# Performance work log

Hardware: AMD Instinct MI355X
Metric: run time of the kernel (lower is better)

Reference implementation:

```python
import jax, jax.numpy as jnp
import numpy as np

VOCAB, EMB, HID = 32000, 512, 1024

def setup_inputs() -> dict:
    key = jax.random.key(0)
    k1, k2, k3, k4, k5, k6 = jax.random.split(key, 6)
    s_e = 1.0 / np.sqrt(EMB)
    s_h = 1.0 / np.sqrt(HID)
    return {
        "x": jax.random.randint(k1, (32, 512), 0, VOCAB, dtype=jnp.int64),
        "emb_table": jax.random.normal(k2, (VOCAB, EMB), dtype=jnp.float32),
        "W_ih": jax.random.uniform(k3, (4 * HID, EMB), jnp.float32, -s_h, s_h),
        "W_hh": jax.random.uniform(k4, (4 * HID, HID), jnp.float32, -s_h, s_h),
        "b_ih": jax.random.uniform(k5, (4 * HID,), jnp.float32, -s_h, s_h),
        "b_hh": jax.random.uniform(k6, (4 * HID,), jnp.float32, -s_h, s_h),
    }

def _lstm(embedded, W_ih, W_hh, b_ih, b_hh):
    # embedded: [B, T, E]; gates order (PyTorch): i, f, g, o
    B = embedded.shape[0]
    H = W_hh.shape[1]
    # Precompute input projections for all timesteps: [B, T, 4H]
    x_proj = jnp.einsum('bte,ge->btg', embedded, W_ih) + b_ih + b_hh

    def step(carry, xt):
        h, c = carry
        gates = xt + h @ W_hh.T  # [B, 4H]
        i, f, g, o = jnp.split(gates, 4, axis=-1)
        i = jax.nn.sigmoid(i)
        f = jax.nn.sigmoid(f)
        g = jnp.tanh(g)
        o = jax.nn.sigmoid(o)
        c = f * c + i * g
        h = o * jnp.tanh(c)
        return (h, c), h

    h0 = jnp.zeros((B, H), embedded.dtype)
    c0 = jnp.zeros((B, H), embedded.dtype)
    (h_f, c_f), hs = jax.lax.scan(step, (h0, c0), jnp.swapaxes(x_proj, 0, 1))
    return jnp.swapaxes(hs, 0, 1), h_f, c_f

def reference(x, emb_table, W_ih, W_hh, b_ih, b_hh):
    embedded = emb_table[x]  # [B, T, E]
    encoder_outputs, state_h, state_c = _lstm(embedded, W_ih, W_hh, b_ih, b_hh)
    return encoder_outputs, state_h, state_c
```

## Files before the change

### kernel.cpp

```cpp
#include <hip/hip_runtime.h>

#define Bb 32
#define Tt 512
#define Ee 512
#define Hh 1024
#define NSLOT 256

typedef __attribute__((ext_vector_type(8))) short bf16x8;
typedef __attribute__((ext_vector_type(4))) float f32x4;
typedef unsigned long long u64;

__device__ __forceinline__ unsigned short f2bf(float f) {
  unsigned int u = __float_as_uint(f);
  u = (u + 0x7fffu + ((u >> 16) & 1u)) >> 16;
  return (unsigned short)u;
}
__device__ __forceinline__ float bf2f(unsigned short s) {
  return __uint_as_float(((unsigned int)s) << 16);
}
__device__ __forceinline__ float sigmoidf_(float x) {
  x = fminf(fmaxf(x, -30.f), 30.f);
  return 1.f / (1.f + __expf(-x));
}
__device__ __forceinline__ float tanh_fast(float x) {
  float xx = fminf(fmaxf(x, -15.f), 15.f);
  float e = __expf(2.f * xx);
  return (e - 1.f) / (e + 1.f);
}

__global__ void gather_kernel(const int* __restrict__ x,
                              const float* __restrict__ emb,
                              unsigned short* __restrict__ emb_hi,
                              unsigned short* __restrict__ emb_lo,
                              unsigned short* __restrict__ hbuf,
                              unsigned* __restrict__ bar) {
  long long gid = (long long)blockIdx.x * blockDim.x + threadIdx.x;
  long long stride = (long long)gridDim.x * blockDim.x;
  for (long long i = gid; i < 8192; i += stride)
    ((ushort4*)hbuf)[i] = make_ushort4(0, 0, 0, 0);
  for (long long i = gid; i < 1024; i += stride)
    bar[i] = 0u;
  long long n4 = (long long)Bb * Tt * Ee / 4;
  for (long long i = gid; i < n4; i += stride) {
    long long bt = i >> 7;
    int e4 = (int)(i & 127);
    int row = x[bt];
    row = min(max(row, 0), 31999);
    float4 v = ((const float4*)(emb + (long long)row * Ee))[e4];
    ushort4 hv, lv;
    hv.x = f2bf(v.x); lv.x = f2bf(v.x - bf2f(hv.x));
    hv.y = f2bf(v.y); lv.y = f2bf(v.y - bf2f(hv.y));
    hv.z = f2bf(v.z); lv.z = f2bf(v.z - bf2f(hv.z));
    hv.w = f2bf(v.w); lv.w = f2bf(v.w - bf2f(hv.w));
    ((ushort4*)emb_hi)[i] = hv;
    ((ushort4*)emb_lo)[i] = lv;
  }
}

__global__ __launch_bounds__(256, 1)
void lstm_kernel(const unsigned short* __restrict__ emb_hi,
                 const unsigned short* __restrict__ emb_lo,
                 unsigned short* __restrict__ hbuf,
                 unsigned* __restrict__ bar,
                 const float* __restrict__ W_ih,
                 const float* __restrict__ W_hh,
                 const float* __restrict__ b_ih,
                 const float* __restrict__ b_hh,
                 float* __restrict__ out) {
  __shared__ unsigned short sWih_hi[16 * 512];
  __shared__ unsigned short sWih_lo[16 * 512];
  __shared__ unsigned short sWhh_hi[16 * 1024];
  __shared__ unsigned short sWhh_lo[16 * 1024];
  __shared__ float sAcc[2][4][2][16][17];
  __shared__ float sBias[16];
  __shared__ float sC[32][4];

  const int tid = threadIdx.x;
  const int lane = tid & 63;
  const int wv = tid >> 6;
  const int wg = blockIdx.x;
  const int j0 = (wg & 7) * 128 + (wg >> 3) * 4;
  const int gflag = (wg & 7) * 4 + (wg >> 6);

  for (int idx = tid; idx < 16 * 64; idx += 256) {
    int c = idx >> 6, kc8 = idx & 63;
    int grow = (c >> 2) * Hh + j0 + (c & 3);
    const float* src = W_ih + (long long)grow * Ee + kc8 * 8;
    int us = (c * 512 + kc8 * 8) ^ ((c & 7) << 3);
#pragma unroll
    for (int j = 0; j < 8; j++) {
      float f = src[j];
      unsigned short h = f2bf(f);
      sWih_hi[us + j] = h;
      sWih_lo[us + j] = f2bf(f - bf2f(h));
    }
  }
  for (int idx = tid; idx < 16 * 128; idx += 256) {
    int c = idx >> 7, kc8 = idx & 127;
    int grow = (c >> 2) * Hh + j0 + (c & 3);
    const float* src = W_hh + (long long)grow * Hh + kc8 * 8;
    int us = (c * 1024 + kc8 * 8) ^ ((c & 7) << 3);
#pragma unroll
    for (int j = 0; j < 8; j++) {
      float f = src[j];
      unsigned short h = f2bf(f);
      sWhh_hi[us + j] = h;
      sWhh_lo[us + j] = f2bf(f - bf2f(h));
    }
  }
  if (tid < 16) {
    int grow = (tid >> 2) * Hh + j0 + (tid & 3);
    sBias[tid] = b_ih[grow] + b_hh[grow];
  }
  if (tid < 128) sC[tid >> 2][tid & 3] = 0.f;
  __syncthreads();

  const int r16 = lane & 15;
  const int kg = (lane >> 4) * 8;
  const int col = lane & 15;
  const int xr = (col & 7) << 3;

  const unsigned* fp = bar + (unsigned)(wv + 4 * (lane & 7)) * 16;

  float h_last = 0.f, c_last = 0.f;

  for (int t = 0; t < Tt; t++) {
    f32x4 acc[2][3];
#pragma unroll
    for (int mt = 0; mt < 2; mt++)
#pragma unroll
      for (int cb = 0; cb < 3; cb++)
        acc[mt][cb] = (f32x4){0.f, 0.f, 0.f, 0.f};

#pragma unroll
    for (int q = 0; q < 4; q++) {
      int kc = wv + q * 4;
      int bo = (col * 512 + kc * 32 + kg) ^ xr;
      bf16x8 bH = *(const bf16x8*)(sWih_hi + bo);
      bf16x8 bL = *(const bf16x8*)(sWih_lo + bo);
#pragma unroll
      for (int mt = 0; mt < 2; mt++) {
        int rb = mt * 16 + r16;
        int ai = (rb * Tt + t) * Ee + kc * 32 + kg;
        bf16x8 aH = *(const bf16x8*)(emb_hi + ai);
        bf16x8 aL = *(const bf16x8*)(emb_lo + ai);
        acc[mt][0] = __builtin_amdgcn_mfma_f32_16x16x32_bf16(aH, bH, acc[mt][0], 0, 0, 0);
        acc[mt][1] = __builtin_amdgcn_mfma_f32_16x16x32_bf16(aH, bL, acc[mt][1], 0, 0, 0);
        acc[mt][2] = __builtin_amdgcn_mfma_f32_16x16x32_bf16(aL, bH, acc[mt][2], 0, 0, 0);
      }
    }

    {
      unsigned target = 16u * (unsigned)t;
      while (__any(__hip_atomic_load(fp, __ATOMIC_RELAXED,
                                     __HIP_MEMORY_SCOPE_AGENT) < target))
        __builtin_amdgcn_s_sleep(1);
    }
    __builtin_amdgcn_sched_barrier(0);

    const unsigned short* hb = hbuf + (unsigned)(t & (NSLOT - 1)) * 32768;
#pragma unroll
    for (int q = 0; q < 8; q++) {
      int kc = wv + q * 4;
      int bo = (col * 1024 + kc * 32 + kg) ^ xr;
      bf16x8 bH = *(const bf16x8*)(sWhh_hi + bo);
      bf16x8 bL = *(const bf16x8*)(sWhh_lo + bo);
#pragma unroll
      for (int mt = 0; mt < 2; mt++) {
        int rb = mt * 16 + r16;
        bf16x8 aH = *(const bf16x8*)(hb + rb * Hh + kc * 32 + kg);
        acc[mt][0] = __builtin_amdgcn_mfma_f32_16x16x32_bf16(aH, bH, acc[mt][0], 0, 0, 0);
        acc[mt][1] = __builtin_amdgcn_mfma_f32_16x16x32_bf16(aH, bL, acc[mt][1], 0, 0, 0);
      }
    }

#pragma unroll
    for (int mt = 0; mt < 2; mt++) {
      f32x4 tot = acc[mt][0] + acc[mt][1] + acc[mt][2];
#pragma unroll
      for (int r = 0; r < 4; r++)
        sAcc[t & 1][wv][mt][(lane >> 4) * 4 + r][col] = tot[r];
    }
    __syncthreads();

    if (tid < 128) {
      int b = tid >> 2, du = tid & 3;
      int mt = b >> 4, rr = b & 15;
      float g0 = sBias[0 * 4 + du], g1 = sBias[1 * 4 + du];
      float g2 = sBias[2 * 4 + du], g3 = sBias[3 * 4 + du];
#pragma unroll
      for (int w = 0; w < 4; w++) {
        g0 += sAcc[t & 1][w][mt][rr][0 * 4 + du];
        g1 += sAcc[t & 1][w][mt][rr][1 * 4 + du];
        g2 += sAcc[t & 1][w][mt][rr][2 * 4 + du];
        g3 += sAcc[t & 1][w][mt][rr][3 * 4 + du];
      }
      float ig = sigmoidf_(g0);
      float fg = sigmoidf_(g1);
      float gg = tanh_fast(g2);
      float og = sigmoidf_(g3);
      float cn = fg * sC[b][du] + ig * gg;
      sC[b][du] = cn;
      float hn = og * tanh_fast(cn);
      h_last = hn; c_last = cn;

      unsigned pack = (unsigned)f2bf(hn);
      unsigned other = __shfl_xor(pack, 1, 64);
      unsigned* nb32 =
          (unsigned*)(hbuf + (unsigned)((t + 1) & (NSLOT - 1)) * 32768);
      if ((du & 1) == 0) {
        unsigned w = (pack & 0xffffu) | (other << 16);
        __hip_atomic_store(nb32 + ((b * 1024 + j0 + du) >> 1), w,
                           __ATOMIC_RELAXED, __HIP_MEMORY_SCOPE_AGENT);
      }
      asm volatile("s_waitcnt vmcnt(0)" ::: "memory");
      if ((tid & 63) == 0)
        __hip_atomic_fetch_add(bar + gflag * 16, 1u, __ATOMIC_RELAXED,
                               __HIP_MEMORY_SCOPE_AGENT);
      out[((long long)b * Tt + t) * Hh + j0 + du] = hn;
    }
  }

  if (tid < 128) {
    int b = tid >> 2, du = tid & 3;
    int hj = j0 + du;
    out[16777216LL + b * Hh + hj] = h_last;
    out[16777216LL + 32768 + b * Hh + hj] = c_last;
  }
}

extern "C" void kernel_launch(void* const* d_in, const int* in_sizes, int n_in,
                              void* d_out, int out_size, void* d_ws, size_t ws_size,
                              hipStream_t stream) {
  const int* x      = (const int*)d_in[0];
  const float* emb  = (const float*)d_in[1];
  const float* W_ih = (const float*)d_in[2];
  const float* W_hh = (const float*)d_in[3];
  const float* b_ih = (const float*)d_in[4];
  const float* b_hh = (const float*)d_in[5];
  float* out = (float*)d_out;

  unsigned short* emb_hi = (unsigned short*)d_ws;
  unsigned short* emb_lo = emb_hi + 8388608;
  unsigned short* hbuf   = emb_lo + 8388608;
  unsigned*       bar    = (unsigned*)(hbuf + 8388608);

  hipLaunchKernelGGL(gather_kernel, dim3(2048), dim3(256), 0, stream,
                     x, emb, emb_hi, emb_lo, hbuf, bar);

  void* args[] = { (void*)&emb_hi, (void*)&emb_lo, (void*)&hbuf, (void*)&bar,
                   (void*)&W_ih, (void*)&W_hh, (void*)&b_ih, (void*)&b_hh,
                   (void*)&out };
  hipLaunchCooperativeKernel((void*)lstm_kernel, dim3(256), dim3(256), args, 0, stream);
}
```

Measured before the change: 3.464 ms.

## Hoist input projection into separate precompute kernel before recurrent LSTM loop

Adds an xproj_kernel that computes the full input projection (embedding times W_ih, three-term bf16 split) for all timesteps into a workspace buffer. The cooperative recurrent kernel then only loads four precomputed gate values per thread per step and runs the W_hh product. This takes the W_ih MFMA work and its shared memory off the serial per-step path. The cost is an extra kernel of only 64 blocks plus a 256 MB fp32 intermediate write and read. A workspace-size check falls back to the original fused kernel when the buffer is too small.

```diff
diff --git a/kernel.cpp b/kernel.cpp
--- a/kernel.cpp
+++ b/kernel.cpp
@@ -58,15 +58,225 @@
 }
 
 __global__ __launch_bounds__(256, 1)
-void lstm_kernel(const unsigned short* __restrict__ emb_hi,
-                 const unsigned short* __restrict__ emb_lo,
-                 unsigned short* __restrict__ hbuf,
+void xproj_kernel(const unsigned short* __restrict__ emb_hi,
+                  const unsigned short* __restrict__ emb_lo,
+                  const float* __restrict__ W_ih,
+                  float* __restrict__ xp) {
+  __shared__ unsigned short sW_hi[64 * 512];
+  __shared__ unsigned short sW_lo[64 * 512];
+  const int tid = threadIdx.x;
+  const int lane = tid & 63;
+  const int wv = tid >> 6;
+  const int p = blockIdx.x;
+
+  for (int idx = tid; idx < 64 * 64; idx += 256) {
+    int c = idx >> 6, k8 = idx & 63;
+    int grow = (c >> 4) * Hh + p * 16 + (c & 15);
+    const float* src = W_ih + (long long)grow * Ee + k8 * 8;
+    int us = (c * 512 + k8 * 8) ^ ((c & 7) << 3);
+#pragma unroll
+    for (int j = 0; j < 8; j++) {
+      float f = src[j];
+      unsigned short h = f2bf(f);
+      sW_hi[us + j] = h;
+      sW_lo[us + j] = f2bf(f - bf2f(h));
+    }
+  }
+  __syncthreads();
+
+  const int r16 = lane & 15;
+  const int kg = (lane >> 4) * 8;
+  const int cB = wv * 16 + (lane & 15);
+  const int xrB = (cB & 7) << 3;
+  const int growc = wv * Hh + p * 16 + (lane & 15);
+
+  for (int t = 0; t < Tt; t++) {
+    f32x4 acc[2][3];
+#pragma unroll
+    for (int mt = 0; mt < 2; mt++)
+#pragma unroll
+      for (int cb = 0; cb < 3; cb++)
+        acc[mt][cb] = (f32x4){0.f, 0.f, 0.f, 0.f};
+#pragma unroll
+    for (int q = 0; q < 16; q++) {
+      int bo = (cB * 512 + q * 32 + kg) ^ xrB;
+      bf16x8 bH = *(const bf16x8*)(sW_hi + bo);
+      bf16x8 bL = *(const bf16x8*)(sW_lo + bo);
+#pragma unroll
+      for (int mt = 0; mt < 2; mt++) {
+        long long ai = ((long long)(mt * 16 + r16) * Tt + t) * Ee + q * 32 + kg;
+        bf16x8 aH = *(const bf16x8*)(emb_hi + ai);
+        bf16x8 aL = *(const bf16x8*)(emb_lo + ai);
+        acc[mt][0] = __builtin_amdgcn_mfma_f32_16x16x32_bf16(aH, bH, acc[mt][0], 0, 0, 0);
+        acc[mt][1] = __builtin_amdgcn_mfma_f32_16x16x32_bf16(aH, bL, acc[mt][1], 0, 0, 0);
+        acc[mt][2] = __builtin_amdgcn_mfma_f32_16x16x32_bf16(aL, bH, acc[mt][2], 0, 0, 0);
+      }
+    }
+#pragma unroll
+    for (int mt = 0; mt < 2; mt++) {
+      f32x4 v = acc[mt][0] + acc[mt][1] + acc[mt][2];
+#pragma unroll
+      for (int r = 0; r < 4; r++) {
+        int b = (lane >> 4) * 4 + r + 16 * mt;
+        xp[((long long)t * Bb + b) * 4096 + growc] = v[r];
+      }
+    }
+  }
+}
+
+__global__ __launch_bounds__(256, 1)
+void lstm_kernel(const unsigned short* __restrict__ hbuf_c,
                  unsigned* __restrict__ bar,
-                 const float* __restrict__ W_ih,
+                 const float* __restrict__ xp,
                  const float* __restrict__ W_hh,
                  const float* __restrict__ b_ih,
                  const float* __restrict__ b_hh,
                  float* __restrict__ out) {
+  __shared__ unsigned short sWhh_hi[16 * 1024];
+  __shared__ unsigned short sWhh_lo[16 * 1024];
+  __shared__ float sAcc[2][4][2][16][17];
+  __shared__ float sBias[16];
+  __shared__ float sC[32][4];
+
+  unsigned short* hbuf = (unsigned short*)hbuf_c;
+  const int tid = threadIdx.x;
+  const int lane = tid & 63;
+  const int wv = tid >> 6;
+  const int wg = blockIdx.x;
+  const int j0 = (wg & 7) * 128 + (wg >> 3) * 4;
+  const int gflag = (wg & 7) * 4 + (wg >> 6);
+
+  for (int idx = tid; idx < 16 * 128; idx += 256) {
+    int c = idx >> 7, kc8 = idx & 127;
+    int grow = (c >> 2) * Hh + j0 + (c & 3);
+    const float* src = W_hh + (long long)grow * Hh + kc8 * 8;
+    int us = (c * 1024 + kc8 * 8) ^ ((c & 7) << 3);
+#pragma unroll
+    for (int j = 0; j < 8; j++) {
+      float f = src[j];
+      unsigned short h = f2bf(f);
+      sWhh_hi[us + j] = h;
+      sWhh_lo[us + j] = f2bf(f - bf2f(h));
+    }
+  }
+  if (tid < 16) {
+    int grow = (tid >> 2) * Hh + j0 + (tid & 3);
+    sBias[tid] = b_ih[grow] + b_hh[grow];
+  }
+  if (tid < 128) sC[tid >> 2][tid & 3] = 0.f;
+  __syncthreads();
+
+  const int r16 = lane & 15;
+  const int kg = (lane >> 4) * 8;
+  const int col = lane & 15;
+  const int xr = (col & 7) << 3;
+  const unsigned* fp = bar + (unsigned)(wv + 4 * (lane & 7)) * 16;
+
+  float h_last = 0.f, c_last = 0.f;
+
+  for (int t = 0; t < Tt; t++) {
+    float xg0 = 0.f, xg1 = 0.f, xg2 = 0.f, xg3 = 0.f;
+    if (tid < 128) {
+      int b = tid >> 2, du = tid & 3;
+      const float* xb = xp + ((long long)t * Bb + b) * 4096 + j0 + du;
+      xg0 = xb[0]; xg1 = xb[1024]; xg2 = xb[2048]; xg3 = xb[3072];
+    }
+
+    {
+      unsigned target = 16u * (unsigned)t;
+      while (__any(__hip_atomic_load(fp, __ATOMIC_RELAXED,
+                                     __HIP_MEMORY_SCOPE_AGENT) < target))
+        __builtin_amdgcn_s_sleep(1);
+    }
+    __builtin_amdgcn_sched_barrier(0);
+
+    const unsigned short* hb = hbuf + (unsigned)(t & (NSLOT - 1)) * 32768;
+    f32x4 acc[2][2];
+#pragma unroll
+    for (int mt = 0; mt < 2; mt++)
+#pragma unroll
+      for (int cb = 0; cb < 2; cb++)
+        acc[mt][cb] = (f32x4){0.f, 0.f, 0.f, 0.f};
+#pragma unroll
+    for (int q = 0; q < 8; q++) {
+      int kc = wv + q * 4;
+      int bo = (col * 1024 + kc * 32 + kg) ^ xr;
+      bf16x8 bH = *(const bf16x8*)(sWhh_hi + bo);
+      bf16x8 bL = *(const bf16x8*)(sWhh_lo + bo);
+#pragma unroll
+      for (int mt = 0; mt < 2; mt++) {
+        int rb = mt * 16 + r16;
+        bf16x8 aH = *(const bf16x8*)(hb + rb * Hh + kc * 32 + kg);
+        acc[mt][0] = __builtin_amdgcn_mfma_f32_16x16x32_bf16(aH, bH, acc[mt][0], 0, 0, 0);
+        acc[mt][1] = __builtin_amdgcn_mfma_f32_16x16x32_bf16(aH, bL, acc[mt][1], 0, 0, 0);
+      }
+    }
+
+#pragma unroll
+    for (int mt = 0; mt < 2; mt++) {
+      f32x4 tot = acc[mt][0] + acc[mt][1];
+#pragma unroll
+      for (int r = 0; r < 4; r++)
+        sAcc[t & 1][wv][mt][(lane >> 4) * 4 + r][col] = tot[r];
+    }
+    __syncthreads();
+
+    if (tid < 128) {
+      int b = tid >> 2, du = tid & 3;
+      int mt = b >> 4, rr = b & 15;
+      float g0 = sBias[0 * 4 + du] + xg0, g1 = sBias[1 * 4 + du] + xg1;
+      float g2 = sBias[2 * 4 + du] + xg2, g3 = sBias[3 * 4 + du] + xg3;
+#pragma unroll
+      for (int w = 0; w < 4; w++) {
+        g0 += sAcc[t & 1][w][mt][rr][0 * 4 + du];
+        g1 += sAcc[t & 1][w][mt][rr][1 * 4 + du];
+        g2 += sAcc[t & 1][w][mt][rr][2 * 4 + du];
+        g3 += sAcc[t & 1][w][mt][rr][3 * 4 + du];
+      }
+      float ig = sigmoidf_(g0);
+      float fg = sigmoidf_(g1);
+      float gg = tanh_fast(g2);
+      float og = sigmoidf_(g3);
+      float cn = fg * sC[b][du] + ig * gg;
+      sC[b][du] = cn;
+      float hn = og * tanh_fast(cn);
+      h_last = hn; c_last = cn;
+
+      unsigned pack = (unsigned)f2bf(hn);
+      unsigned other = __shfl_xor(pack, 1, 64);
+      unsigned* nb32 =
+          (unsigned*)(hbuf + (unsigned)((t + 1) & (NSLOT - 1)) * 32768);
+      if ((du & 1) == 0) {
+        unsigned w = (pack & 0xffffu) | (other << 16);
+        __hip_atomic_store(nb32 + ((b * 1024 + j0 + du) >> 1), w,
+                           __ATOMIC_RELAXED, __HIP_MEMORY_SCOPE_AGENT);
+      }
+      asm volatile("s_waitcnt vmcnt(0)" ::: "memory");
+      if ((tid & 63) == 0)
+        __hip_atomic_fetch_add(bar + gflag * 16, 1u, __ATOMIC_RELAXED,
+                               __HIP_MEMORY_SCOPE_AGENT);
+      out[((long long)b * Tt + t) * Hh + j0 + du] = hn;
+    }
+  }
+
+  if (tid < 128) {
+    int b = tid >> 2, du = tid & 3;
+    int hj = j0 + du;
+    out[16777216LL + b * Hh + hj] = h_last;
+    out[16777216LL + 32768 + b * Hh + hj] = c_last;
+  }
+}
+
+__global__ __launch_bounds__(256, 1)
+void lstm_kernel_fb(const unsigned short* __restrict__ emb_hi,
+                    const unsigned short* __restrict__ emb_lo,
+                    unsigned short* __restrict__ hbuf,
+                    unsigned* __restrict__ bar,
+                    const float* __restrict__ W_ih,
+                    const float* __restrict__ W_hh,
+                    const float* __restrict__ b_ih,
+                    const float* __restrict__ b_hh,
+                    float* __restrict__ out) {
   __shared__ unsigned short sWih_hi[16 * 512];
   __shared__ unsigned short sWih_lo[16 * 512];
   __shared__ unsigned short sWhh_hi[16 * 1024];
@@ -119,7 +329,6 @@
   const int kg = (lane >> 4) * 8;
   const int col = lane & 15;
   const int xr = (col & 7) << 3;
-
   const unsigned* fp = bar + (unsigned)(wv + 4 * (lane & 7)) * 16;
 
   float h_last = 0.f, c_last = 0.f;
@@ -131,7 +340,6 @@
 #pragma unroll
       for (int cb = 0; cb < 3; cb++)
         acc[mt][cb] = (f32x4){0.f, 0.f, 0.f, 0.f};
-
 #pragma unroll
     for (int q = 0; q < 4; q++) {
       int kc = wv + q * 4;
@@ -149,7 +357,6 @@
         acc[mt][2] = __builtin_amdgcn_mfma_f32_16x16x32_bf16(aL, bH, acc[mt][2], 0, 0, 0);
       }
     }
-
     {
       unsigned target = 16u * (unsigned)t;
       while (__any(__hip_atomic_load(fp, __ATOMIC_RELAXED,
@@ -157,7 +364,6 @@
         __builtin_amdgcn_s_sleep(1);
     }
     __builtin_amdgcn_sched_barrier(0);
-
     const unsigned short* hb = hbuf + (unsigned)(t & (NSLOT - 1)) * 32768;
 #pragma unroll
     for (int q = 0; q < 8; q++) {
@@ -173,7 +379,6 @@
         acc[mt][1] = __builtin_amdgcn_mfma_f32_16x16x32_bf16(aH, bL, acc[mt][1], 0, 0, 0);
       }
     }
-
 #pragma unroll
     for (int mt = 0; mt < 2; mt++) {
       f32x4 tot = acc[mt][0] + acc[mt][1] + acc[mt][2];
@@ -182,7 +387,6 @@
         sAcc[t & 1][wv][mt][(lane >> 4) * 4 + r][col] = tot[r];
     }
     __syncthreads();
-
     if (tid < 128) {
       int b = tid >> 2, du = tid & 3;
       int mt = b >> 4, rr = b & 15;
@@ -203,7 +407,6 @@
       sC[b][du] = cn;
       float hn = og * tanh_fast(cn);
       h_last = hn; c_last = cn;
-
       unsigned pack = (unsigned)f2bf(hn);
       unsigned other = __shfl_xor(pack, 1, 64);
       unsigned* nb32 =
@@ -220,7 +423,6 @@
       out[((long long)b * Tt + t) * Hh + j0 + du] = hn;
     }
   }
-
   if (tid < 128) {
     int b = tid >> 2, du = tid & 3;
     int hj = j0 + du;
@@ -244,12 +446,23 @@
   unsigned short* emb_lo = emb_hi + 8388608;
   unsigned short* hbuf   = emb_lo + 8388608;
   unsigned*       bar    = (unsigned*)(hbuf + 8388608);
+  float*          xp     = (float*)((char*)d_ws + 50335744);
 
   hipLaunchKernelGGL(gather_kernel, dim3(2048), dim3(256), 0, stream,
                      x, emb, emb_hi, emb_lo, hbuf, bar);
 
-  void* args[] = { (void*)&emb_hi, (void*)&emb_lo, (void*)&hbuf, (void*)&bar,
-                   (void*)&W_ih, (void*)&W_hh, (void*)&b_ih, (void*)&b_hh,
-                   (void*)&out };
-  hipLaunchCooperativeKernel((void*)lstm_kernel, dim3(256), dim3(256), args, 0, stream);
-}
+  if (ws_size >= 318771200ull) {
+    hipLaunchKernelGGL(xproj_kernel, dim3(64), dim3(256), 0, stream,
+                       emb_hi, emb_lo, W_ih, xp);
+    void* args[] = { (void*)&hbuf, (void*)&bar, (void*)&xp,
+                     (void*)&W_hh, (void*)&b_ih, (void*)&b_hh, (void*)&out };
+    hipLaunchCooperativeKernel((void*)lstm_kernel, dim3(256), dim3(256),
+                               args, 0, stream);
+  } else {
+    void* args[] = { (void*)&emb_hi, (void*)&emb_lo, (void*)&hbuf, (void*)&bar,
+                     (void*)&W_ih, (void*)&W_hh, (void*)&b_ih, (void*)&b_hh,
+                     (void*)&out };
+    hipLaunchCooperativeKernel((void*)lstm_kernel_fb, dim3(256), dim3(256),
+                               args, 0, stream);
+  }
+}
```

Result: no change. 3.459 ms (-0.1%).

## Replace counter barrier with sentinel-tagged hidden-state buffer polling

Applied to the files above, without the earlier changes.

Removes the per-step atomic counter barrier and instead fills a full-length (non-ring) hidden-state buffer with a NaN sentinel, so consumers poll the data itself until no sentinel remains. Hidden-state loads are issued early at the start of each step, overlapping with the input-projection MFMAs. This removes the vmcnt wait and the fetch_add round trip on the producer side, but the gather kernel now has to write a much larger sentinel-initialised buffer, and correctness depends on no computed h value ever encoding to the sentinel bit pattern and on 64-bit loads not tearing.

```diff
diff --git a/kernel.cpp b/kernel.cpp
--- a/kernel.cpp
+++ b/kernel.cpp
@@ -4,11 +4,13 @@
 #define Tt 512
 #define Ee 512
 #define Hh 1024
-#define NSLOT 256
 
 typedef __attribute__((ext_vector_type(8))) short bf16x8;
 typedef __attribute__((ext_vector_type(4))) float f32x4;
+typedef __attribute__((ext_vector_type(4))) unsigned u32x4;
 typedef unsigned long long u64;
+
+#define SEN 0x7FC0u
 
 __device__ __forceinline__ unsigned short f2bf(float f) {
   unsigned int u = __float_as_uint(f);
@@ -32,14 +34,15 @@
                               const float* __restrict__ emb,
                               unsigned short* __restrict__ emb_hi,
                               unsigned short* __restrict__ emb_lo,
-                              unsigned short* __restrict__ hbuf,
-                              unsigned* __restrict__ bar) {
+                              unsigned short* __restrict__ hbuf) {
   long long gid = (long long)blockIdx.x * blockDim.x + threadIdx.x;
   long long stride = (long long)gridDim.x * blockDim.x;
   for (long long i = gid; i < 8192; i += stride)
     ((ushort4*)hbuf)[i] = make_ushort4(0, 0, 0, 0);
-  for (long long i = gid; i < 1024; i += stride)
-    bar[i] = 0u;
+  for (long long i = 8192 + gid; i < 4194304; i += stride)
+    ((ushort4*)hbuf)[i] =
+        make_ushort4((unsigned short)SEN, (unsigned short)SEN,
+                     (unsigned short)SEN, (unsigned short)SEN);
   long long n4 = (long long)Bb * Tt * Ee / 4;
   for (long long i = gid; i < n4; i += stride) {
     long long bt = i >> 7;
@@ -61,7 +64,6 @@
 void lstm_kernel(const unsigned short* __restrict__ emb_hi,
                  const unsigned short* __restrict__ emb_lo,
                  unsigned short* __restrict__ hbuf,
-                 unsigned* __restrict__ bar,
                  const float* __restrict__ W_ih,
                  const float* __restrict__ W_hh,
                  const float* __restrict__ b_ih,
@@ -80,7 +82,6 @@
   const int wv = tid >> 6;
   const int wg = blockIdx.x;
   const int j0 = (wg & 7) * 128 + (wg >> 3) * 4;
-  const int gflag = (wg & 7) * 4 + (wg >> 6);
 
   for (int idx = tid; idx < 16 * 64; idx += 256) {
     int c = idx >> 6, kc8 = idx & 63;
@@ -120,18 +121,30 @@
   const int col = lane & 15;
   const int xr = (col & 7) << 3;
 
-  const unsigned* fp = bar + (unsigned)(wv + 4 * (lane & 7)) * 16;
-
   float h_last = 0.f, c_last = 0.f;
 
   for (int t = 0; t < Tt; t++) {
+    __builtin_amdgcn_sched_barrier(0);
+
+    const u32x4* hb4 = (const u32x4*)(hbuf + (u64)t * 32768);
+    const u64* hb8 = (const u64*)(hbuf + (u64)t * 32768);
+    u32x4 hA[8], hB[8];
+    int iA[8], iB[8];
+#pragma unroll
+    for (int q = 0; q < 8; q++) {
+      int kc = wv + q * 4;
+      iA[q] = (r16 * Hh + kc * 32 + kg) >> 3;
+      iB[q] = ((16 + r16) * Hh + kc * 32 + kg) >> 3;
+      hA[q] = hb4[iA[q]];
+      hB[q] = hb4[iB[q]];
+    }
+
     f32x4 acc[2][3];
 #pragma unroll
     for (int mt = 0; mt < 2; mt++)
 #pragma unroll
       for (int cb = 0; cb < 3; cb++)
         acc[mt][cb] = (f32x4){0.f, 0.f, 0.f, 0.f};
-
 #pragma unroll
     for (int q = 0; q < 4; q++) {
       int kc = wv + q * 4;
@@ -150,28 +163,54 @@
       }
     }
 
-    {
-      unsigned target = 16u * (unsigned)t;
-      while (__any(__hip_atomic_load(fp, __ATOMIC_RELAXED,
-                                     __HIP_MEMORY_SCOPE_AGENT) < target))
-        __builtin_amdgcn_s_sleep(1);
-    }
-    __builtin_amdgcn_sched_barrier(0);
-
-    const unsigned short* hb = hbuf + (unsigned)(t & (NSLOT - 1)) * 32768;
 #pragma unroll
     for (int q = 0; q < 8; q++) {
       int kc = wv + q * 4;
+      {
+        u32x4 v = hA[q];
+        bool bad = ((v[0] & 0xFFFFu) == SEN) | ((v[1] & 0xFFFFu) == SEN) |
+                   ((v[2] & 0xFFFFu) == SEN) | ((v[3] & 0xFFFFu) == SEN);
+        while (__any(bad)) {
+          if (bad) {
+            u64 lo = __hip_atomic_load(hb8 + iA[q] * 2, __ATOMIC_RELAXED,
+                                       __HIP_MEMORY_SCOPE_AGENT);
+            u64 hi = __hip_atomic_load(hb8 + iA[q] * 2 + 1, __ATOMIC_RELAXED,
+                                       __HIP_MEMORY_SCOPE_AGENT);
+            v[0] = (unsigned)lo; v[1] = (unsigned)(lo >> 32);
+            v[2] = (unsigned)hi; v[3] = (unsigned)(hi >> 32);
+          }
+          bad = ((v[0] & 0xFFFFu) == SEN) | ((v[1] & 0xFFFFu) == SEN) |
+                ((v[2] & 0xFFFFu) == SEN) | ((v[3] & 0xFFFFu) == SEN);
+        }
+        hA[q] = v;
+      }
+      {
+        u32x4 v = hB[q];
+        bool bad = ((v[0] & 0xFFFFu) == SEN) | ((v[1] & 0xFFFFu) == SEN) |
+                   ((v[2] & 0xFFFFu) == SEN) | ((v[3] & 0xFFFFu) == SEN);
+        while (__any(bad)) {
+          if (bad) {
+            u64 lo = __hip_atomic_load(hb8 + iB[q] * 2, __ATOMIC_RELAXED,
+                                       __HIP_MEMORY_SCOPE_AGENT);
+            u64 hi = __hip_atomic_load(hb8 + iB[q] * 2 + 1, __ATOMIC_RELAXED,
+                                       __HIP_MEMORY_SCOPE_AGENT);
+            v[0] = (unsigned)lo; v[1] = (unsigned)(lo >> 32);
+            v[2] = (unsigned)hi; v[3] = (unsigned)(hi >> 32);
+          }
+          bad = ((v[0] & 0xFFFFu) == SEN) | ((v[1] & 0xFFFFu) == SEN) |
+                ((v[2] & 0xFFFFu) == SEN) | ((v[3] & 0xFFFFu) == SEN);
+        }
+        hB[q] = v;
+      }
+      union { u32x4 u; bf16x8 v; } ua, ub;
+      ua.u = hA[q]; ub.u = hB[q];
       int bo = (col * 1024 + kc * 32 + kg) ^ xr;
       bf16x8 bH = *(const bf16x8*)(sWhh_hi + bo);
       bf16x8 bL = *(const bf16x8*)(sWhh_lo + bo);
-#pragma unroll
-      for (int mt = 0; mt < 2; mt++) {
-        int rb = mt * 16 + r16;
-        bf16x8 aH = *(const bf16x8*)(hb + rb * Hh + kc * 32 + kg);
-        acc[mt][0] = __builtin_amdgcn_mfma_f32_16x16x32_bf16(aH, bH, acc[mt][0], 0, 0, 0);
-        acc[mt][1] = __builtin_amdgcn_mfma_f32_16x16x32_bf16(aH, bL, acc[mt][1], 0, 0, 0);
-      }
+      acc[0][0] = __builtin_amdgcn_mfma_f32_16x16x32_bf16(ua.v, bH, acc[0][0], 0, 0, 0);
+      acc[0][1] = __builtin_amdgcn_mfma_f32_16x16x32_bf16(ua.v, bL, acc[0][1], 0, 0, 0);
+      acc[1][0] = __builtin_amdgcn_mfma_f32_16x16x32_bf16(ub.v, bH, acc[1][0], 0, 0, 0);
+      acc[1][1] = __builtin_amdgcn_mfma_f32_16x16x32_bf16(ub.v, bL, acc[1][1], 0, 0, 0);
     }
 
 #pragma unroll
@@ -206,17 +245,12 @@
 
       unsigned pack = (unsigned)f2bf(hn);
       unsigned other = __shfl_xor(pack, 1, 64);
-      unsigned* nb32 =
-          (unsigned*)(hbuf + (unsigned)((t + 1) & (NSLOT - 1)) * 32768);
-      if ((du & 1) == 0) {
+      if (t + 1 < Tt && (du & 1) == 0) {
         unsigned w = (pack & 0xffffu) | (other << 16);
+        unsigned* nb32 = (unsigned*)(hbuf + (u64)(t + 1) * 32768);
         __hip_atomic_store(nb32 + ((b * 1024 + j0 + du) >> 1), w,
                            __ATOMIC_RELAXED, __HIP_MEMORY_SCOPE_AGENT);
       }
-      asm volatile("s_waitcnt vmcnt(0)" ::: "memory");
-      if ((tid & 63) == 0)
-        __hip_atomic_fetch_add(bar + gflag * 16, 1u, __ATOMIC_RELAXED,
-                               __HIP_MEMORY_SCOPE_AGENT);
       out[((long long)b * Tt + t) * Hh + j0 + du] = hn;
     }
   }
@@ -243,12 +277,11 @@
   unsigned short* emb_hi = (unsigned short*)d_ws;
   unsigned short* emb_lo = emb_hi + 8388608;
   unsigned short* hbuf   = emb_lo + 8388608;
-  unsigned*       bar    = (unsigned*)(hbuf + 8388608);
 
   hipLaunchKernelGGL(gather_kernel, dim3(2048), dim3(256), 0, stream,
-                     x, emb, emb_hi, emb_lo, hbuf, bar);
-
-  void* args[] = { (void*)&emb_hi, (void*)&emb_lo, (void*)&hbuf, (void*)&bar,
+                     x, emb, emb_hi, emb_lo, hbuf);
+
+  void* args[] = { (void*)&emb_hi, (void*)&emb_lo, (void*)&hbuf,
                    (void*)&W_ih, (void*)&W_hh, (void*)&b_ih, (void*)&b_hh,
                    (void*)&out };
   hipLaunchCooperativeKernel((void*)lstm_kernel, dim3(256), dim3(256), args, 0, stream);
```

Result: faster. 3.124 ms (-9.8%).
